# Kernel tuning notes

Hardware: AMD Instinct MI355X
Metric: run time of the kernel (lower is better)

Reference implementation:

```python
import jax, jax.numpy as jnp
import numpy as np

# dims
B, L, DIN = 32, 1024, 8
D, KK, S = 128, 16, 8
K = (L - KK) // S + 1  # 127 patch tokens
NB, F = 4, 24
Q = 256.0  # Q8.8 scale


def _ste(x, y):
    # straight-through: forward = y (quantized), backward = identity
    return x + jax.lax.stop_gradient(y - x)


def q88(x):
    q = jnp.clip(jnp.round(x * Q), -32768.0, 32767.0) / Q
    return _ste(x, q)


def sig_lut(x):
    xq = q88(x)
    return q88(jax.nn.sigmoid(xq))


def silu_lut(x):
    xq = q88(x)
    return q88(xq * jax.nn.sigmoid(xq))


def layernorm(x, g, b, eps=1e-5):
    m = jnp.mean(x, axis=-1, keepdims=True)
    v = jnp.mean((x - m) ** 2, axis=-1, keepdims=True)
    return (x - m) * jax.lax.rsqrt(v + eps) * g + b


def conv1x1_q88(x, w, b):
    # x: (B, Cin, L); w: (Cout, Cin); Q8.8 integer-emulated pointwise conv
    y = jnp.einsum('bcl,oc->bol', q88(x), q88(w)) + q88(b)[None, :, None]
    return q88(y)


def conv1d_q88(x, w, b, stride):
    # x: (B, Cin, L); w: (Cout, Cin, k)
    y = jax.lax.conv_general_dilated(q88(x), q88(w), (stride,), 'VALID',
                                     dimension_numbers=('NCH', 'OIH', 'NCH'))
    return q88(y + q88(b)[None, :, None])


def ssm_scan(x, w_dt, b_dt):
    # x: (B, K, D). dt_proj acts along the time axis (Linear K->K), per source.
    # lam_all[b,t,d] = sigmoid_LUT(sum_k x[b,k,d] * w_dt[t,k] + b_dt[t])
    lam = sig_lut(jnp.einsum('bkd,tk->btd', x, w_dt) + b_dt[None, :, None])
    xs = jnp.moveaxis(x, 1, 0)      # (K, B, D)
    lams = jnp.moveaxis(lam, 1, 0)  # (K, B, D)

    def step(s, tu):
        lam_t, u_t = tu
        s = lam_t * s + (1.0 - lam_t) * u_t
        return s, s

    s0 = jnp.zeros(x.shape[::2], dtype=x.dtype)  # (B, D)
    _, ys = jax.lax.scan(step, s0, (lams, xs))
    return jnp.moveaxis(ys, 0, 1)  # (B, K, D)


def setup_inputs() -> dict:
    key = jax.random.key(0)
    ks = jax.random.split(key, 20)
    n = lambda k, sh, s=0.05: (jax.random.normal(k, sh, dtype=jnp.float32) * s)
    return {
        'x': jax.random.normal(ks[0], (B, L, DIN), dtype=jnp.float32),
        'w_proj': n(ks[1], (D, DIN), 0.2), 'b_proj': n(ks[2], (D,), 0.02),
        'w_patch': n(ks[3], (D, D, KK), 0.05), 'b_patch': n(ks[4], (D,), 0.02),
        'pe': n(ks[5], (K, D), 0.5), 'pe_scale': jnp.float32(1.0),
        'ln_g': jnp.ones((NB, D), jnp.float32), 'ln_b': jnp.zeros((NB, D), jnp.float32),
        'w_in': n(ks[6], (NB, D, D), 0.08), 'w_gate': n(ks[7], (NB, D, D), 0.08),
        'w_out': n(ks[8], (NB, D, D), 0.08),
        'w_dt': n(ks[9], (NB, K, K), 0.08), 'b_dt': n(ks[10], (NB, K), 0.02),
        'lnf_g': jnp.ones((D,), jnp.float32), 'lnf_b': jnp.zeros((D,), jnp.float32),
        'w_flat': n(ks[11], (D * F, D, K), 0.02), 'b_flat': n(ks[12], (D * F,), 0.02),
        'w_head': n(ks[13], (2, D), 0.1), 'b_head': n(ks[14], (2,), 0.02),
    }


def reference(x, w_proj, b_proj, w_patch, b_patch, pe, pe_scale,
              ln_g, ln_b, w_in, w_gate, w_out, w_dt, b_dt,
              lnf_g, lnf_b, w_flat, b_flat, w_head, b_head):
    xc = jnp.transpose(x, (0, 2, 1))                # (B, DIN, L)
    xp = conv1x1_q88(xc, w_proj, b_proj)            # (B, D, L)
    xe = conv1d_q88(xp, w_patch, b_patch, S)        # (B, D, K)
    h = jnp.transpose(xe, (0, 2, 1)) + pe_scale * pe[None]  # (B, K, D)
    for i in range(NB):
        hn = layernorm(h, ln_g[i], ln_b[i])
        u = silu_lut(jnp.einsum('bkd,de->bke', hn, w_in[i]))
        y = ssm_scan(u, w_dt[i], b_dt[i])
        g = silu_lut(jnp.einsum('bkd,de->bke', hn, w_gate[i]))
        h = h + jnp.einsum('bkd,de->bke', y * g, w_out[i])
    h = layernorm(h, lnf_g, lnf_b)
    xp2 = jnp.transpose(h, (0, 2, 1))               # (B, D, K)
    # output_layer_flat: full-length Conv1d kernel==K -> one giant contraction
    y_feat = q88(jnp.einsum('bdk,odk->bo', q88(xp2), q88(w_flat)) + q88(b_flat))
    y_feat = y_feat.reshape(x.shape[0], D, F)       # (B, D, F)
    out = conv1x1_q88(y_feat, w_head, b_head)       # (B, 2, F)
    return out
```

## Files before the change

### kernel.cpp

```cpp
#include <hip/hip_runtime.h>
#include <cmath>

#define DEV __device__ __forceinline__

namespace {

constexpr int Kp    = 127;
constexpr int Mrows = 32 * Kp;
constexpr int Rred  = 128 * Kp;

DEV float q88(float x) {
  float r = rintf(x * 256.0f);
  r = fminf(fmaxf(r, -32768.0f), 32767.0f);
  return r * 0.00390625f;
}
DEV float sigmoid_(float x) { return 1.0f / (1.0f + expf(-x)); }

DEV void fma16(const float4 av, const float4 bv, float (&acc)[4][4]) {
  acc[0][0] = fmaf(av.x, bv.x, acc[0][0]); acc[0][1] = fmaf(av.x, bv.y, acc[0][1]);
  acc[0][2] = fmaf(av.x, bv.z, acc[0][2]); acc[0][3] = fmaf(av.x, bv.w, acc[0][3]);
  acc[1][0] = fmaf(av.y, bv.x, acc[1][0]); acc[1][1] = fmaf(av.y, bv.y, acc[1][1]);
  acc[1][2] = fmaf(av.y, bv.z, acc[1][2]); acc[1][3] = fmaf(av.y, bv.w, acc[1][3]);
  acc[2][0] = fmaf(av.z, bv.x, acc[2][0]); acc[2][1] = fmaf(av.z, bv.y, acc[2][1]);
  acc[2][2] = fmaf(av.z, bv.z, acc[2][2]); acc[2][3] = fmaf(av.z, bv.w, acc[2][3]);
  acc[3][0] = fmaf(av.w, bv.x, acc[3][0]); acc[3][1] = fmaf(av.w, bv.y, acc[3][1]);
  acc[3][2] = fmaf(av.w, bv.z, acc[3][2]); acc[3][3] = fmaf(av.w, bv.w, acc[3][3]);
}

__global__ __launch_bounds__(256) void k_quant(
    const float* __restrict__ wproj, const float* __restrict__ bproj,
    const float* __restrict__ wpatch, const float* __restrict__ bpatch,
    const float* __restrict__ whead, const float* __restrict__ bhead,
    const float* __restrict__ bflat,
    float* __restrict__ wq_proj, float* __restrict__ bq_proj, float* __restrict__ wpq,
    float* __restrict__ bq_patch, float* __restrict__ wq_head, float* __restrict__ bq_head,
    float* __restrict__ bq_flat) {
  int i = blockIdx.x * 256 + threadIdx.x;
  if (i < 262144) {
    int j = i >> 14;
    int c = (i >> 7) & 127;
    int d = i & 127;
    wpq[i] = q88(wpatch[(d * 128 + c) * 16 + j]);
  }
  int t = i - 262144;
  if (t >= 0) {
    if      (t < 1024) wq_proj[t]         = q88(wproj[t]);
    else if (t < 1152) bq_proj[t - 1024]  = q88(bproj[t - 1024]);
    else if (t < 1280) bq_patch[t - 1152] = q88(bpatch[t - 1152]);
    else if (t < 1536) wq_head[t - 1280]  = q88(whead[t - 1280]);
    else if (t < 1538) bq_head[t - 1536]  = q88(bhead[t - 1536]);
    else if (t < 4610) bq_flat[t - 1538]  = q88(bflat[t - 1538]);
  }
}

__global__ __launch_bounds__(256) void k_proj(const float* __restrict__ x, const float* __restrict__ wq,
                                              const float* __restrict__ bq, float* __restrict__ xpq) {
  int bl0 = blockIdx.x * 16;
  int tid = threadIdx.x;
  __shared__ float xs[128];
  if (tid < 128) xs[tid] = q88(x[(size_t)bl0 * 8 + tid]);
  __syncthreads();
  int o = tid & 127;
  int half = tid >> 7;
  float wv[8];
#pragma unroll
  for (int c = 0; c < 8; ++c) wv[c] = wq[o * 8 + c];
  float bb = bq[o];
#pragma unroll
  for (int il = 0; il < 8; ++il) {
    int l_loc = half * 8 + il;
    float acc = bb;
#pragma unroll
    for (int c = 0; c < 8; ++c) acc = fmaf(xs[l_loc * 8 + c], wv[c], acc);
    xpq[(size_t)(bl0 + l_loc) * 128 + o] = q88(acc);
  }
}

__global__ __launch_bounds__(256) void k_patch(const float* __restrict__ xpq, const float* __restrict__ wpq,
                                               float* __restrict__ partJ) {
  __shared__ __align__(16) float As[128][36];
  int mt = blockIdx.x, jg = blockIdx.y;
  int tid = threadIdx.x;
  int mr = tid & 31, c0 = (tid >> 5) * 16;
  int tn = tid & 31, tm8 = tid >> 5;
  int m0 = mt * 32;
  int g = m0 + mr;
  int bb = g / 127, kq = g % 127;
  float acc[4][4] = {};
  for (int jj = 0; jj < 4; ++jj) {
    int j = jg * 4 + jj;
    const float* src = xpq + ((size_t)bb * 1024 + kq * 8 + j) * 128 + c0;
    __syncthreads();
#pragma unroll
    for (int q = 0; q < 4; ++q) {
      float4 v = *reinterpret_cast<const float4*>(src + q * 4);
      As[c0 + q * 4 + 0][mr] = v.x;
      As[c0 + q * 4 + 1][mr] = v.y;
      As[c0 + q * 4 + 2][mr] = v.z;
      As[c0 + q * 4 + 3][mr] = v.w;
    }
    __syncthreads();
    const float* wp = wpq + (size_t)j * 16384 + tn * 4;
#pragma unroll 4
    for (int c = 0; c < 128; ++c) {
      float4 bv = *reinterpret_cast<const float4*>(wp + c * 128);
      float4 av = *reinterpret_cast<const float4*>(&As[c][tm8 * 4]);
      fma16(av, bv, acc);
    }
  }
  float* dst = partJ + ((size_t)jg * Mrows + m0) * 128 + tn * 4;
#pragma unroll
  for (int i = 0; i < 4; ++i) {
    float4 o4 = make_float4(acc[i][0], acc[i][1], acc[i][2], acc[i][3]);
    *reinterpret_cast<float4*>(dst + (size_t)(tm8 * 4 + i) * 128) = o4;
  }
}

__global__ __launch_bounds__(256) void k_combine(const float* __restrict__ partJ, const float* __restrict__ bqp,
                                                 const float* __restrict__ pe, const float* __restrict__ pesc,
                                                 float* __restrict__ h) {
  int i = blockIdx.x * 256 + threadIdx.x;
  int n = i & 127;
  int gq = i >> 7;
  int k = gq % 127;
  float s = partJ[i] + partJ[520192 + i] + partJ[2 * 520192 + i] + partJ[3 * 520192 + i] + bqp[n];
  h[i] = q88(s) + pesc[0] * pe[k * 128 + n];
}

__global__ __launch_bounds__(256) void k_ln_ug(const float* __restrict__ h, const float* __restrict__ lng,
                                               const float* __restrict__ lnb, const float* __restrict__ Win,
                                               const float* __restrict__ Wgate, float* __restrict__ u,
                                               float* __restrict__ gbuf) {
  __shared__ __align__(16) float As[128][36];
  __shared__ float2 lnpart[8][32];
  __shared__ float mean_s[32], inv_s[32];
  const float* W = blockIdx.y ? Wgate : Win;
  float* out = blockIdx.y ? gbuf : u;
  int tid = threadIdx.x;
  int mr = tid & 31, c0 = (tid >> 5) * 16;
  int m0 = blockIdx.x * 32;
  const float* src = h + (size_t)(m0 + mr) * 128 + c0;
  float s1 = 0.f, s2 = 0.f;
#pragma unroll
  for (int q = 0; q < 4; ++q) {
    float4 v = *reinterpret_cast<const float4*>(src + q * 4);
    As[c0 + q * 4 + 0][mr] = v.x;
    As[c0 + q * 4 + 1][mr] = v.y;
    As[c0 + q * 4 + 2][mr] = v.z;
    As[c0 + q * 4 + 3][mr] = v.w;
    s1 += v.x + v.y + v.z + v.w;
    s2 = fmaf(v.x, v.x, s2); s2 = fmaf(v.y, v.y, s2);
    s2 = fmaf(v.z, v.z, s2); s2 = fmaf(v.w, v.w, s2);
  }
  lnpart[tid >> 5][mr] = make_float2(s1, s2);
  __syncthreads();
  if (tid < 32) {
    float s = 0.f, ss = 0.f;
#pragma unroll
    for (int j = 0; j < 8; ++j) { float2 p = lnpart[j][tid]; s += p.x; ss += p.y; }
    float mn = s * (1.0f / 128.0f);
    float var = ss * (1.0f / 128.0f) - mn * mn;
    mean_s[tid] = mn;
    inv_s[tid] = rsqrtf(var + 1e-5f);
  }
  __syncthreads();
  float mnv = mean_s[mr], invv = inv_s[mr];
#pragma unroll
  for (int q = 0; q < 16; ++q) {
    int c = c0 + q;
    As[c][mr] = (As[c][mr] - mnv) * invv * lng[c] + lnb[c];
  }
  __syncthreads();
  int tn = tid & 31, tm8 = tid >> 5;
  float acc[4][4] = {};
  const float* wp = W + tn * 4;
#pragma unroll 4
  for (int c = 0; c < 128; ++c) {
    float4 bv = *reinterpret_cast<const float4*>(wp + c * 128);
    float4 av = *reinterpret_cast<const float4*>(&As[c][tm8 * 4]);
    fma16(av, bv, acc);
  }
  float* dst = out + (size_t)m0 * 128 + tn * 4;
#pragma unroll
  for (int i = 0; i < 4; ++i) {
    float4 o4;
    { float xq = q88(acc[i][0]); o4.x = q88(xq * sigmoid_(xq)); }
    { float xq = q88(acc[i][1]); o4.y = q88(xq * sigmoid_(xq)); }
    { float xq = q88(acc[i][2]); o4.z = q88(xq * sigmoid_(xq)); }
    { float xq = q88(acc[i][3]); o4.w = q88(xq * sigmoid_(xq)); }
    *reinterpret_cast<float4*>(dst + (size_t)(tm8 * 4 + i) * 128) = o4;
  }
}

__global__ __launch_bounds__(128) void k_lam(const float* __restrict__ u, const float* __restrict__ wdt,
                                             const float* __restrict__ bdt, float* __restrict__ lam) {
  int blk = blockIdx.x;
  int b = blk / 127, t = blk % 127;
  int d = threadIdx.x;
  __shared__ float wr[127];
  if (d < 127) wr[d] = wdt[t * 127 + d];
  __syncthreads();
  const float* up = u + (size_t)b * (127 * 128) + d;
  float acc = 0.f;
#pragma unroll 4
  for (int k = 0; k < 127; ++k) acc = fmaf(up[(size_t)k * 128], wr[k], acc);
  float pre = q88(acc + bdt[t]);
  lam[((size_t)b * 127 + t) * 128 + d] = q88(sigmoid_(pre));
}

__global__ __launch_bounds__(256) void k_scan(const float* __restrict__ u, const float* __restrict__ gbuf,
                                              float* __restrict__ lamp) {
  int gt = blockIdx.x * 256 + threadIdx.x;
  int b = gt >> 7, d = gt & 127;
  size_t base = (size_t)b * (127 * 128) + d;
  float s = 0.f;
  for (int t = 0; t < 127; ++t) {
    size_t idx = base + (size_t)t * 128;
    float lm = lamp[idx];
    float uu = u[idx];
    s = lm * s + (1.0f - lm) * uu;
    lamp[idx] = s * gbuf[idx];
  }
}

__global__ __launch_bounds__(256) void k_outproj(const float* __restrict__ p, const float* __restrict__ W,
                                                 float* __restrict__ h) {
  __shared__ __align__(16) float As[128][36];
  int tid = threadIdx.x;
  int mr = tid & 31, c0 = (tid >> 5) * 16;
  int m0 = blockIdx.x * 32;
  const float* src = p + (size_t)(m0 + mr) * 128 + c0;
#pragma unroll
  for (int q = 0; q < 4; ++q) {
    float4 v = *reinterpret_cast<const float4*>(src + q * 4);
    As[c0 + q * 4 + 0][mr] = v.x;
    As[c0 + q * 4 + 1][mr] = v.y;
    As[c0 + q * 4 + 2][mr] = v.z;
    As[c0 + q * 4 + 3][mr] = v.w;
  }
  __syncthreads();
  int tn = tid & 31, tm8 = tid >> 5;
  float acc[4][4] = {};
  const float* wp = W + tn * 4;
#pragma unroll 4
  for (int c = 0; c < 128; ++c) {
    float4 bv = *reinterpret_cast<const float4*>(wp + c * 128);
    float4 av = *reinterpret_cast<const float4*>(&As[c][tm8 * 4]);
    fma16(av, bv, acc);
  }
  float* dst = h + (size_t)m0 * 128 + tn * 4;
#pragma unroll
  for (int i = 0; i < 4; ++i) {
    float4 hv = *reinterpret_cast<float4*>(dst + (size_t)(tm8 * 4 + i) * 128);
    hv.x += acc[i][0]; hv.y += acc[i][1]; hv.z += acc[i][2]; hv.w += acc[i][3];
    *reinterpret_cast<float4*>(dst + (size_t)(tm8 * 4 + i) * 128) = hv;
  }
}

__global__ __launch_bounds__(128) void k_lnf(const float* __restrict__ h, const float* __restrict__ gg,
                                             const float* __restrict__ bb, float* __restrict__ xp2q) {
  int row = blockIdx.x;
  int d = threadIdx.x;
  float v = h[(size_t)row * 128 + d];
  __shared__ float red[128];
  __shared__ float mn_s, inv_s;
  red[d] = v;
  __syncthreads();
  for (int off = 64; off > 0; off >>= 1) {
    if (d < off) red[d] += red[d + off];
    __syncthreads();
  }
  if (d == 0) mn_s = red[0] * (1.0f / 128.0f);
  __syncthreads();
  float dv = v - mn_s;
  red[d] = dv * dv;
  __syncthreads();
  for (int off = 64; off > 0; off >>= 1) {
    if (d < off) red[d] += red[d + off];
    __syncthreads();
  }
  if (d == 0) inv_s = rsqrtf(red[0] * (1.0f / 128.0f) + 1e-5f);
  __syncthreads();
  float hn = (v - mn_s) * inv_s * gg[d] + bb[d];
  int b = row / 127, k = row % 127;
  xp2q[((size_t)b * 128 + d) * 127 + k] = q88(hn);
}

__global__ __launch_bounds__(128) void k_flat(const float* __restrict__ Aq, const float* __restrict__ Wf,
                                              float* __restrict__ partF) {
  constexpr int RC = 32;
  __shared__ __align__(16) float As[RC][36];
  __shared__ __align__(16) float Ws[RC][132];
  int ot = blockIdx.x, rs = blockIdx.y;
  int tid = threadIdx.x;
  int og = tid & 31;
  int bg = tid >> 5;
  int o0 = ot * 128;
  int r0 = rs * 512;
  float acc[8][4] = {};
  for (int ch = 0; ch < 512; ch += RC) {
    int rbase = r0 + ch;
    __syncthreads();
    {
      int r = tid & 31;
      int b = tid >> 5;
      int rr = rbase + r;
      bool ok = rr < Rred;
#pragma unroll
      for (int q = 0; q < 8; ++q) {
        int bb2 = b + 4 * q;
        As[r][bb2] = ok ? Aq[(size_t)bb2 * Rred + rr] : 0.f;
      }
    }
    {
      int r = tid & 31;
      int oo = tid >> 5;
      int rr = rbase + r;
      size_t rcl = (rr < Rred) ? (size_t)rr : (size_t)(Rred - 1);
#pragma unroll 8
      for (int q = 0; q < 32; ++q) {
        int o = oo + 4 * q;
        Ws[r][o] = q88(Wf[(size_t)(o0 + o) * Rred + rcl]);
      }
    }
    __syncthreads();
#pragma unroll 4
    for (int r = 0; r < RC; ++r) {
      float4 w  = *reinterpret_cast<const float4*>(&Ws[r][og * 4]);
      float4 a0 = *reinterpret_cast<const float4*>(&As[r][bg * 8]);
      float4 a1 = *reinterpret_cast<const float4*>(&As[r][bg * 8 + 4]);
      acc[0][0] = fmaf(a0.x, w.x, acc[0][0]); acc[0][1] = fmaf(a0.x, w.y, acc[0][1]);
      acc[0][2] = fmaf(a0.x, w.z, acc[0][2]); acc[0][3] = fmaf(a0.x, w.w, acc[0][3]);
      acc[1][0] = fmaf(a0.y, w.x, acc[1][0]); acc[1][1] = fmaf(a0.y, w.y, acc[1][1]);
      acc[1][2] = fmaf(a0.y, w.z, acc[1][2]); acc[1][3] = fmaf(a0.y, w.w, acc[1][3]);
      acc[2][0] = fmaf(a0.z, w.x, acc[2][0]); acc[2][1] = fmaf(a0.z, w.y, acc[2][1]);
      acc[2][2] = fmaf(a0.z, w.z, acc[2][2]); acc[2][3] = fmaf(a0.z, w.w, acc[2][3]);
      acc[3][0] = fmaf(a0.w, w.x, acc[3][0]); acc[3][1] = fmaf(a0.w, w.y, acc[3][1]);
      acc[3][2] = fmaf(a0.w, w.z, acc[3][2]); acc[3][3] = fmaf(a0.w, w.w, acc[3][3]);
      acc[4][0] = fmaf(a1.x, w.x, acc[4][0]); acc[4][1] = fmaf(a1.x, w.y, acc[4][1]);
      acc[4][2] = fmaf(a1.x, w.z, acc[4][2]); acc[4][3] = fmaf(a1.x, w.w, acc[4][3]);
      acc[5][0] = fmaf(a1.y, w.x, acc[5][0]); acc[5][1] = fmaf(a1.y, w.y, acc[5][1]);
      acc[5][2] = fmaf(a1.y, w.z, acc[5][2]); acc[5][3] = fmaf(a1.y, w.w, acc[5][3]);
      acc[6][0] = fmaf(a1.z, w.x, acc[6][0]); acc[6][1] = fmaf(a1.z, w.y, acc[6][1]);
      acc[6][2] = fmaf(a1.z, w.z, acc[6][2]); acc[6][3] = fmaf(a1.z, w.w, acc[6][3]);
      acc[7][0] = fmaf(a1.w, w.x, acc[7][0]); acc[7][1] = fmaf(a1.w, w.y, acc[7][1]);
      acc[7][2] = fmaf(a1.w, w.z, acc[7][2]); acc[7][3] = fmaf(a1.w, w.w, acc[7][3]);
    }
  }
#pragma unroll
  for (int bi = 0; bi < 8; ++bi) {
    int b = bg * 8 + bi;
    float4 o4 = make_float4(acc[bi][0], acc[bi][1], acc[bi][2], acc[bi][3]);
    *reinterpret_cast<float4*>(partF + ((size_t)rs * 32 + b) * 3072 + o0 + og * 4) = o4;
  }
}

__global__ __launch_bounds__(256) void k_head(const float* __restrict__ partF, const float* __restrict__ bqf,
                                              const float* __restrict__ wqh, const float* __restrict__ bqh,
                                              float* __restrict__ out) {
  int b = blockIdx.x;
  int tid = threadIdx.x;
  __shared__ float yf[3072];
#pragma unroll
  for (int i = 0; i < 12; ++i) {
    int o = tid + 256 * i;
    float s = bqf[o];
    for (int rsq = 0; rsq < 32; ++rsq) s += partF[((size_t)rsq * 32 + b) * 3072 + o];
    yf[o] = q88(s);
  }
  __syncthreads();
  if (tid < 48) {
    int oh = tid / 24, f = tid % 24;
    float acc = bqh[oh];
    for (int d = 0; d < 128; ++d) acc = fmaf(yf[d * 24 + f], wqh[oh * 128 + d], acc);
    out[(size_t)b * 48 + oh * 24 + f] = q88(acc);
  }
}

}

extern "C" void kernel_launch(void* const* d_in, const int* in_sizes, int n_in,
                              void* d_out, int out_size, void* d_ws, size_t ws_size,
                              hipStream_t stream) {
  const float* x      = (const float*)d_in[0];
  const float* wproj  = (const float*)d_in[1];
  const float* bproj  = (const float*)d_in[2];
  const float* wpatch = (const float*)d_in[3];
  const float* bpatch = (const float*)d_in[4];
  const float* pe     = (const float*)d_in[5];
  const float* pescal = (const float*)d_in[6];
  const float* lng    = (const float*)d_in[7];
  const float* lnb    = (const float*)d_in[8];
  const float* win    = (const float*)d_in[9];
  const float* wgate  = (const float*)d_in[10];
  const float* wout   = (const float*)d_in[11];
  const float* wdt    = (const float*)d_in[12];
  const float* bdt    = (const float*)d_in[13];
  const float* lnfg   = (const float*)d_in[14];
  const float* lnfb   = (const float*)d_in[15];
  const float* wflat  = (const float*)d_in[16];
  const float* bflat  = (const float*)d_in[17];
  const float* whead  = (const float*)d_in[18];
  const float* bhead  = (const float*)d_in[19];
  float* out = (float*)d_out;
  float* ws  = (float*)d_ws;

  constexpr size_t O_WQPROJ  = 0;
  constexpr size_t O_BQPROJ  = 1024;
  constexpr size_t O_WPQ     = 2048;
  constexpr size_t O_BQPATCH = 264192;
  constexpr size_t O_WQHEAD  = 264320;
  constexpr size_t O_BQHEAD  = 264576;
  constexpr size_t O_BQFLAT  = 264704;
  constexpr size_t O_XPQ     = 267776;
  constexpr size_t O_PARTJ   = 4462080;
  constexpr size_t O_H       = 6542848;
  constexpr size_t O_U       = 7063040;
  constexpr size_t O_G       = 7583232;
  constexpr size_t O_LAMP    = 8103424;
  constexpr size_t O_XP2Q    = 8623616;
  constexpr size_t O_PARTF   = O_XPQ;

  k_quant<<<(262144 + 4610 + 255) / 256, 256, 0, stream>>>(
      wproj, bproj, wpatch, bpatch, whead, bhead, bflat,
      ws + O_WQPROJ, ws + O_BQPROJ, ws + O_WPQ, ws + O_BQPATCH,
      ws + O_WQHEAD, ws + O_BQHEAD, ws + O_BQFLAT);

  k_proj<<<2048, 256, 0, stream>>>(x, ws + O_WQPROJ, ws + O_BQPROJ, ws + O_XPQ);

  {
    dim3 g(127, 4);
    k_patch<<<g, 256, 0, stream>>>(ws + O_XPQ, ws + O_WPQ, ws + O_PARTJ);
  }
  k_combine<<<2032, 256, 0, stream>>>(ws + O_PARTJ, ws + O_BQPATCH, pe, pescal, ws + O_H);

  for (int i = 0; i < 4; ++i) {
    dim3 g4(127, 2);
    k_ln_ug<<<g4, 256, 0, stream>>>(ws + O_H, lng + i * 128, lnb + i * 128,
                                    win + (size_t)i * 16384, wgate + (size_t)i * 16384,
                                    ws + O_U, ws + O_G);
    k_lam<<<4064, 128, 0, stream>>>(ws + O_U, wdt + (size_t)i * 16129, bdt + (size_t)i * 127,
                                    ws + O_LAMP);
    k_scan<<<16, 256, 0, stream>>>(ws + O_U, ws + O_G, ws + O_LAMP);
    k_outproj<<<127, 256, 0, stream>>>(ws + O_LAMP, wout + (size_t)i * 16384, ws + O_H);
  }

  k_lnf<<<4064, 128, 0, stream>>>(ws + O_H, lnfg, lnfb, ws + O_XP2Q);

  {
    dim3 g(24, 32);
    k_flat<<<g, 128, 0, stream>>>(ws + O_XP2Q, wflat, ws + O_PARTF);
  }
  k_head<<<32, 256, 0, stream>>>(ws + O_PARTF, ws + O_BQFLAT, ws + O_WQHEAD, ws + O_BQHEAD, out);
}
```

Baseline: 449.6 us.

## Tile lambda projection as GEMM, vectorize scan, restructure flat contraction

The per-(b,t) dot-product lambda kernel becomes a shared-memory tiled GEMM with a 4x4 register block per thread. The scan now handles four channels per thread with float4 loads, which also means fewer threads. The flat contraction streams the big weight matrix straight into registers with double-buffered float4 loads, uses an 8x8 accumulator tile, and doubles the split-K count. To make weight quantization a plain rint, the activation is scaled by 1/256 and the weight quantization clamp is dropped. The doubled split-K also doubles the partial-sum buffer and the reduction work in the head kernel, and per-thread row-strided weight loads may coalesce less well.

Result: slower. 765.7 us (+70.3%).

```diff
diff --git a/kernel.cpp b/kernel.cpp
--- a/kernel.cpp
+++ b/kernel.cpp
@@ -192,34 +192,79 @@
   }
 }
 
-__global__ __launch_bounds__(128) void k_lam(const float* __restrict__ u, const float* __restrict__ wdt,
-                                             const float* __restrict__ bdt, float* __restrict__ lam) {
-  int blk = blockIdx.x;
-  int b = blk / 127, t = blk % 127;
-  int d = threadIdx.x;
-  __shared__ float wr[127];
-  if (d < 127) wr[d] = wdt[t * 127 + d];
-  __syncthreads();
-  const float* up = u + (size_t)b * (127 * 128) + d;
-  float acc = 0.f;
+__global__ __launch_bounds__(256) void k_lamg(const float* __restrict__ u, const float* __restrict__ wdt,
+                                              const float* __restrict__ bdt, float* __restrict__ lam) {
+  __shared__ __align__(16) float Wk[32][36];
+  __shared__ __align__(16) float Us[32][132];
+  int b = blockIdx.x, tt = blockIdx.y;
+  int t0 = tt * 32;
+  int tid = threadIdx.x;
+  int dg = tid & 31, tg = tid >> 5;
+  float acc[4][4] = {};
+  const float* ub = u + (size_t)b * (127 * 128);
+  for (int k0 = 0; k0 < 127; k0 += 32) {
+    __syncthreads();
+    {
+      int k = tid & 31, tl = tid >> 5;
+#pragma unroll
+      for (int q = 0; q < 4; ++q) {
+        int t = tl + 8 * q;
+        int tg2 = t0 + t, kg = k0 + k;
+        float v = (tg2 < 127 && kg < 127) ? wdt[tg2 * 127 + kg] : 0.f;
+        Wk[k][t] = v;
+      }
+    }
+    {
+      int dq = tid & 7, k = tid >> 3;
+      int kg = k0 + k;
+      const float* srcp = ub + (size_t)kg * 128 + dq * 16;
+#pragma unroll
+      for (int q = 0; q < 4; ++q) {
+        float4 v = make_float4(0.f, 0.f, 0.f, 0.f);
+        if (kg < 127) v = *reinterpret_cast<const float4*>(srcp + q * 4);
+        *reinterpret_cast<float4*>(&Us[k][dq * 16 + q * 4]) = v;
+      }
+    }
+    __syncthreads();
 #pragma unroll 4
-  for (int k = 0; k < 127; ++k) acc = fmaf(up[(size_t)k * 128], wr[k], acc);
-  float pre = q88(acc + bdt[t]);
-  lam[((size_t)b * 127 + t) * 128 + d] = q88(sigmoid_(pre));
-}
-
-__global__ __launch_bounds__(256) void k_scan(const float* __restrict__ u, const float* __restrict__ gbuf,
+    for (int k = 0; k < 32; ++k) {
+      float4 tv = *reinterpret_cast<const float4*>(&Wk[k][tg * 4]);
+      float4 dv = *reinterpret_cast<const float4*>(&Us[k][dg * 4]);
+      fma16(tv, dv, acc);
+    }
+  }
+#pragma unroll
+  for (int ti = 0; ti < 4; ++ti) {
+    int t = t0 + tg * 4 + ti;
+    if (t < 127) {
+      float bb = bdt[t];
+      float4 o4;
+      o4.x = q88(sigmoid_(q88(acc[ti][0] + bb)));
+      o4.y = q88(sigmoid_(q88(acc[ti][1] + bb)));
+      o4.z = q88(sigmoid_(q88(acc[ti][2] + bb)));
+      o4.w = q88(sigmoid_(q88(acc[ti][3] + bb)));
+      *reinterpret_cast<float4*>(lam + ((size_t)b * 127 + t) * 128 + dg * 4) = o4;
+    }
+  }
+}
+
+__global__ __launch_bounds__(128) void k_scan(const float* __restrict__ u, const float* __restrict__ gbuf,
                                               float* __restrict__ lamp) {
-  int gt = blockIdx.x * 256 + threadIdx.x;
-  int b = gt >> 7, d = gt & 127;
-  size_t base = (size_t)b * (127 * 128) + d;
-  float s = 0.f;
+  int gt = blockIdx.x * 128 + threadIdx.x;
+  int b = gt >> 5, d4 = (gt & 31) * 4;
+  size_t base = (size_t)b * (127 * 128) + d4;
+  float4 s = make_float4(0.f, 0.f, 0.f, 0.f);
   for (int t = 0; t < 127; ++t) {
     size_t idx = base + (size_t)t * 128;
-    float lm = lamp[idx];
-    float uu = u[idx];
-    s = lm * s + (1.0f - lm) * uu;
-    lamp[idx] = s * gbuf[idx];
+    float4 lm = *reinterpret_cast<const float4*>(lamp + idx);
+    float4 uu = *reinterpret_cast<const float4*>(u + idx);
+    float4 gg = *reinterpret_cast<const float4*>(gbuf + idx);
+    s.x = lm.x * s.x + (1.0f - lm.x) * uu.x;
+    s.y = lm.y * s.y + (1.0f - lm.y) * uu.y;
+    s.z = lm.z * s.z + (1.0f - lm.z) * uu.z;
+    s.w = lm.w * s.w + (1.0f - lm.w) * uu.w;
+    float4 p = make_float4(s.x * gg.x, s.y * gg.y, s.z * gg.z, s.w * gg.w);
+    *reinterpret_cast<float4*>(lamp + idx) = p;
   }
 }
 
@@ -286,72 +331,77 @@
   xp2q[((size_t)b * 128 + d) * 127 + k] = q88(hn);
 }
 
-__global__ __launch_bounds__(128) void k_flat(const float* __restrict__ Aq, const float* __restrict__ Wf,
-                                              float* __restrict__ partF) {
-  constexpr int RC = 32;
-  __shared__ __align__(16) float As[RC][36];
-  __shared__ __align__(16) float Ws[RC][132];
+__global__ __launch_bounds__(64) void k_flat(const float* __restrict__ Aq, const float* __restrict__ Wf,
+                                             float* __restrict__ partF) {
+  __shared__ float As[32][32];
   int ot = blockIdx.x, rs = blockIdx.y;
   int tid = threadIdx.x;
-  int og = tid & 31;
-  int bg = tid >> 5;
+  int og = tid & 15, bg = tid >> 4;
   int o0 = ot * 128;
-  int r0 = rs * 512;
-  float acc[8][4] = {};
-  for (int ch = 0; ch < 512; ch += RC) {
-    int rbase = r0 + ch;
-    __syncthreads();
-    {
-      int r = tid & 31;
-      int b = tid >> 5;
-      int rr = rbase + r;
-      bool ok = rr < Rred;
-#pragma unroll
-      for (int q = 0; q < 8; ++q) {
-        int bb2 = b + 4 * q;
-        As[r][bb2] = ok ? Aq[(size_t)bb2 * Rred + rr] : 0.f;
+  int r0 = rs * 256;
+  float acc[8][8] = {};
+  size_t orow[8];
+#pragma unroll
+  for (int i = 0; i < 8; ++i) orow[i] = (size_t)(o0 + og * 8 + i) * Rred;
+
+  float4 wbuf[2][8];
+  {
+    int rc = r0; if (rc > Rred - 4) rc = Rred - 4;
+#pragma unroll
+    for (int i = 0; i < 8; ++i)
+      wbuf[0][i] = *reinterpret_cast<const float4*>(Wf + orow[i] + rc);
+  }
+
+  int sb = tid >> 1, srq = tid & 1;
+  for (int ch = 0; ch < 256; ch += 32) {
+    int rb = r0 + ch;
+    __syncthreads();
+#pragma unroll
+    for (int q = 0; q < 4; ++q) {
+      int rl = srq * 16 + q * 4;
+      int rr = rb + rl;
+      float4 v = make_float4(0.f, 0.f, 0.f, 0.f);
+      if (rr < Rred) v = *reinterpret_cast<const float4*>(Aq + (size_t)sb * Rred + rr);
+      As[rl + 0][sb] = v.x * 0.00390625f;
+      As[rl + 1][sb] = v.y * 0.00390625f;
+      As[rl + 2][sb] = v.z * 0.00390625f;
+      As[rl + 3][sb] = v.w * 0.00390625f;
+    }
+    __syncthreads();
+#pragma unroll
+    for (int qd = 0; qd < 8; ++qd) {
+      int rnext = rb + (qd + 1) * 4;
+      bool more = (ch + 32 < 256) || (qd < 7);
+      if (more) {
+        int rc = rnext; if (rc > Rred - 4) rc = Rred - 4;
+#pragma unroll
+        for (int i = 0; i < 8; ++i)
+          wbuf[(qd + 1) & 1][i] = *reinterpret_cast<const float4*>(Wf + orow[i] + rc);
       }
-    }
-    {
-      int r = tid & 31;
-      int oo = tid >> 5;
-      int rr = rbase + r;
-      size_t rcl = (rr < Rred) ? (size_t)rr : (size_t)(Rred - 1);
-#pragma unroll 8
-      for (int q = 0; q < 32; ++q) {
-        int o = oo + 4 * q;
-        Ws[r][o] = q88(Wf[(size_t)(o0 + o) * Rred + rcl]);
+#pragma unroll
+      for (int j = 0; j < 4; ++j) {
+        int rl = qd * 4 + j;
+        float4 a0 = *reinterpret_cast<const float4*>(&As[rl][bg * 8]);
+        float4 a1 = *reinterpret_cast<const float4*>(&As[rl][bg * 8 + 4]);
+        float a[8] = {a0.x, a0.y, a0.z, a0.w, a1.x, a1.y, a1.z, a1.w};
+#pragma unroll
+        for (int i = 0; i < 8; ++i) {
+          float4 wv = wbuf[qd & 1][i];
+          float w = (j == 0) ? wv.x : (j == 1) ? wv.y : (j == 2) ? wv.z : wv.w;
+          float wq = rintf(w * 256.0f);
+#pragma unroll
+          for (int bi = 0; bi < 8; ++bi)
+            acc[bi][i] = fmaf(a[bi], wq, acc[bi][i]);
+        }
       }
-    }
-    __syncthreads();
-#pragma unroll 4
-    for (int r = 0; r < RC; ++r) {
-      float4 w  = *reinterpret_cast<const float4*>(&Ws[r][og * 4]);
-      float4 a0 = *reinterpret_cast<const float4*>(&As[r][bg * 8]);
-      float4 a1 = *reinterpret_cast<const float4*>(&As[r][bg * 8 + 4]);
-      acc[0][0] = fmaf(a0.x, w.x, acc[0][0]); acc[0][1] = fmaf(a0.x, w.y, acc[0][1]);
-      acc[0][2] = fmaf(a0.x, w.z, acc[0][2]); acc[0][3] = fmaf(a0.x, w.w, acc[0][3]);
-      acc[1][0] = fmaf(a0.y, w.x, acc[1][0]); acc[1][1] = fmaf(a0.y, w.y, acc[1][1]);
-      acc[1][2] = fmaf(a0.y, w.z, acc[1][2]); acc[1][3] = fmaf(a0.y, w.w, acc[1][3]);
-      acc[2][0] = fmaf(a0.z, w.x, acc[2][0]); acc[2][1] = fmaf(a0.z, w.y, acc[2][1]);
-      acc[2][2] = fmaf(a0.z, w.z, acc[2][2]); acc[2][3] = fmaf(a0.z, w.w, acc[2][3]);
-      acc[3][0] = fmaf(a0.w, w.x, acc[3][0]); acc[3][1] = fmaf(a0.w, w.y, acc[3][1]);
-      acc[3][2] = fmaf(a0.w, w.z, acc[3][2]); acc[3][3] = fmaf(a0.w, w.w, acc[3][3]);
-      acc[4][0] = fmaf(a1.x, w.x, acc[4][0]); acc[4][1] = fmaf(a1.x, w.y, acc[4][1]);
-      acc[4][2] = fmaf(a1.x, w.z, acc[4][2]); acc[4][3] = fmaf(a1.x, w.w, acc[4][3]);
-      acc[5][0] = fmaf(a1.y, w.x, acc[5][0]); acc[5][1] = fmaf(a1.y, w.y, acc[5][1]);
-      acc[5][2] = fmaf(a1.y, w.z, acc[5][2]); acc[5][3] = fmaf(a1.y, w.w, acc[5][3]);
-      acc[6][0] = fmaf(a1.z, w.x, acc[6][0]); acc[6][1] = fmaf(a1.z, w.y, acc[6][1]);
-      acc[6][2] = fmaf(a1.z, w.z, acc[6][2]); acc[6][3] = fmaf(a1.z, w.w, acc[6][3]);
-      acc[7][0] = fmaf(a1.w, w.x, acc[7][0]); acc[7][1] = fmaf(a1.w, w.y, acc[7][1]);
-      acc[7][2] = fmaf(a1.w, w.z, acc[7][2]); acc[7][3] = fmaf(a1.w, w.w, acc[7][3]);
     }
   }
 #pragma unroll
   for (int bi = 0; bi < 8; ++bi) {
     int b = bg * 8 + bi;
-    float4 o4 = make_float4(acc[bi][0], acc[bi][1], acc[bi][2], acc[bi][3]);
-    *reinterpret_cast<float4*>(partF + ((size_t)rs * 32 + b) * 3072 + o0 + og * 4) = o4;
+    float* dst = partF + ((size_t)rs * 32 + b) * 3072 + o0 + og * 8;
+    *reinterpret_cast<float4*>(dst)     = make_float4(acc[bi][0], acc[bi][1], acc[bi][2], acc[bi][3]);
+    *reinterpret_cast<float4*>(dst + 4) = make_float4(acc[bi][4], acc[bi][5], acc[bi][6], acc[bi][7]);
   }
 }
 
@@ -365,7 +415,7 @@
   for (int i = 0; i < 12; ++i) {
     int o = tid + 256 * i;
     float s = bqf[o];
-    for (int rsq = 0; rsq < 32; ++rsq) s += partF[((size_t)rsq * 32 + b) * 3072 + o];
+    for (int rsq = 0; rsq < 64; ++rsq) s += partF[((size_t)rsq * 32 + b) * 3072 + o];
     yf[o] = q88(s);
   }
   __syncthreads();
@@ -439,17 +489,20 @@
     k_ln_ug<<<g4, 256, 0, stream>>>(ws + O_H, lng + i * 128, lnb + i * 128,
                                     win + (size_t)i * 16384, wgate + (size_t)i * 16384,
                                     ws + O_U, ws + O_G);
-    k_lam<<<4064, 128, 0, stream>>>(ws + O_U, wdt + (size_t)i * 16129, bdt + (size_t)i * 127,
-                                    ws + O_LAMP);
-    k_scan<<<16, 256, 0, stream>>>(ws + O_U, ws + O_G, ws + O_LAMP);
+    {
+      dim3 gl(32, 4);
+      k_lamg<<<gl, 256, 0, stream>>>(ws + O_U, wdt + (size_t)i * 16129, bdt + (size_t)i * 127,
+                                     ws + O_LAMP);
+    }
+    k_scan<<<8, 128, 0, stream>>>(ws + O_U, ws + O_G, ws + O_LAMP);
     k_outproj<<<127, 256, 0, stream>>>(ws + O_LAMP, wout + (size_t)i * 16384, ws + O_H);
   }
 
   k_lnf<<<4064, 128, 0, stream>>>(ws + O_H, lnfg, lnfb, ws + O_XP2Q);
 
   {
-    dim3 g(24, 32);
-    k_flat<<<g, 128, 0, stream>>>(ws + O_XP2Q, wflat, ws + O_PARTF);
+    dim3 g(24, 64);
+    k_flat<<<g, 64, 0, stream>>>(ws + O_XP2Q, wflat, ws + O_PARTF);
   }
   k_head<<<32, 256, 0, stream>>>(ws + O_PARTF, ws + O_BQFLAT, ws + O_WQHEAD, ws + O_BQHEAD, out);
 }
```
